# Optimization experiments

Hardware: AMD Instinct MI355X
Metric: run time of the kernel (lower is better)

The kernel has to match this reference:

```python
import jax, jax.numpy as jnp
import numpy as np

B, N, DIN, DOUT, T = 16384, 128, 64, 64, 16

def setup_inputs() -> dict:
    key = jax.random.key(0)
    k1, k2, k3, k4, k5 = jax.random.split(key, 5)
    input = jax.random.normal(k1, (B, N, DIN), dtype=jnp.float32)
    g = jax.random.uniform(k2, (N, N), dtype=jnp.float32)
    weight = jax.random.normal(k3, (T, DOUT, DIN), dtype=jnp.float32) * (1.0 / np.sqrt(DIN))
    bias = jax.random.normal(k4, (DOUT,), dtype=jnp.float32) * 0.01
    node_type_index = jax.random.randint(k5, (N,), 0, T, dtype=jnp.int32)
    return {"input": input, "g": g, "weight": weight, "bias": bias,
            "node_type_index": node_type_index}

def reference(input, g, weight, bias, node_type_index):
    # gather per-node weight: [N, out, in]
    w = weight[node_type_index]
    # per-node linear: input [B,N,in] x w [N,out,in] -> [B,N,out]
    h = jnp.einsum('bni,noi->bno', input, w)
    # graph aggregation: g [N,N] @ h -> [B,N,out]
    out = jnp.einsum('nm,bmo->bno', g, h)
    return out + bias
```

## Files before the change

### kernel.cpp

```cpp
#include <hip/hip_runtime.h>
#include <hip/hip_bf16.h>


#define NN   128
#define DI   64
#define DOUT 64
#define TT   16
#define NG   24
#define NCH  32

typedef __attribute__((ext_vector_type(4))) float f32x4;
typedef __attribute__((ext_vector_type(8))) short bf16x8;

__device__ __forceinline__ short f2bf(float f) {
    return __builtin_bit_cast(short, __float2bfloat16(f));
}

__device__ __forceinline__ bf16x8 cvt8(f32x4 a, f32x4 b) {
    bf16x8 r;
    r[0] = f2bf(a[0]); r[1] = f2bf(a[1]); r[2] = f2bf(a[2]); r[3] = f2bf(a[3]);
    r[4] = f2bf(b[0]); r[5] = f2bf(b[1]); r[6] = f2bf(b[2]); r[7] = f2bf(b[3]);
    return r;
}

__device__ __forceinline__ void load_lds16(const float* gp, float* lp) {
    __builtin_amdgcn_global_load_lds(
        (const __attribute__((address_space(1))) unsigned int*)gp,
        (__attribute__((address_space(3))) unsigned int*)lp, 16, 0, 0);
}

__device__ short d_wb[TT * DOUT * DI];
__device__ short d_gb[NN * NN];
__device__ int   d_gp[NG * 8];

__global__ void prep_kernel(const float* __restrict__ weight,
                            const float* __restrict__ g,
                            const int*   __restrict__ ntype) {
    const int tid    = blockIdx.x * blockDim.x + threadIdx.x;
    const int stride = gridDim.x * blockDim.x;
    for (int i = tid; i < TT * DOUT * DI; i += stride) d_wb[i] = f2bf(weight[i]);
    for (int i = tid; i < NN * NN; i += stride)        d_gb[i] = f2bf(g[i]);

    if (blockIdx.x == 0) {
        __shared__ int sh_t[NN];
        const int lt = threadIdx.x;
        if (lt < NN) sh_t[lt] = ntype[lt];
        __syncthreads();
        if (lt < TT) {
            int cnt = 0, m0 = 0;
            for (int m = NN - 1; m >= 0; --m)
                if (sh_t[m] == lt) { ++cnt; m0 = m; }
            const int ng = (cnt + 15) >> 4;
            int pfx = 0, total = 0;
            for (int t2 = 0; t2 < TT; ++t2) {
                const int v = __shfl(ng, t2, 64);
                if (t2 < lt) pfx += v;
                total += v;
            }
            const int fill = m0 * 0x01010101;
            int Gw = pfx, cur = 0, saved = 0;
            int pk[4] = {fill, fill, fill, fill};
            int gf[4] = {fill, fill, fill, fill};
            for (int m = 0; m < NN; ++m) {
                if (sh_t[m] == lt) {
                    const int w2 = cur >> 2, s8 = (cur & 3) * 8;
                    pk[w2] = (pk[w2] & ~(0xFF << s8)) | (m << s8);
                    if (++cur == 16) {
                        for (int k2 = 0; k2 < 4; ++k2) d_gp[Gw * 8 + k2] = pk[k2];
                        d_gp[Gw * 8 + 4] = lt;
                        if (!saved) { for (int k2 = 0; k2 < 4; ++k2) gf[k2] = pk[k2]; saved = 1; }
                        ++Gw; cur = 0;
                        for (int k2 = 0; k2 < 4; ++k2) pk[k2] = fill;
                    }
                }
            }
            if (cur > 0) {
                for (int k2 = 0; k2 < 4; ++k2) d_gp[Gw * 8 + k2] = pk[k2];
                d_gp[Gw * 8 + 4] = lt;
                if (!saved) { for (int k2 = 0; k2 < 4; ++k2) gf[k2] = pk[k2]; saved = 1; }
                ++Gw;
            }
            const unsigned long long msk = __ballot(ng > 0);
            if (lt == __ffsll(msk) - 1) {
                for (int gp2 = total; gp2 < NG; ++gp2) {
                    for (int k2 = 0; k2 < 4; ++k2) d_gp[gp2 * 8 + k2] = gf[k2];
                    d_gp[gp2 * 8 + 4] = lt;
                }
            }
        }
    }
}

__global__ __launch_bounds__(512, 2)
void graph_linear_main(const float* __restrict__ input,
                       const float* __restrict__ bias,
                       float* __restrict__ out)
{
    __shared__ float ibuf0[NN * DI];
    __shared__ float ibuf1[NN * DI];
    __shared__ short hbuf0[DOUT * NN];
    __shared__ short hbuf1[DOUT * NN];

    const int tid  = threadIdx.x;
    const int lane = tid & 63;
    const int wave = tid >> 6;
    const int lo   = lane & 15;
    const int hi   = lane >> 4;
    const size_t bbase = (size_t)blockIdx.x * NCH;
    const float* const inblk = input + bbase * (NN * DI);

    const int wu = __builtin_amdgcn_readfirstlane(wave);
    int mp[NG / 8][5];
#pragma unroll
    for (int it = 0; it < NG / 8; ++it) {
        const int gb = (it * 8 + wu) * 8;
#pragma unroll
        for (int k2 = 0; k2 < 5; ++k2) mp[it][k2] = d_gp[gb + k2];
    }
    bf16x8 wfr[NG / 8][8];
#pragma unroll
    for (int it = 0; it < NG / 8; ++it) {
        const short* wrow = d_wb + mp[it][4] * (DOUT * DI);
#pragma unroll
        for (int ot = 0; ot < 4; ++ot) {
            wfr[it][2 * ot]     = *(const bf16x8*)(wrow + (ot * 16 + lo) * DI + hi * 8);
            wfr[it][2 * ot + 1] = *(const bf16x8*)(wrow + (ot * 16 + lo) * DI + 32 + hi * 8);
        }
    }
    const int n2 = wave * 16 + lo;
    bf16x8 gfr[4];
#pragma unroll
    for (int cc = 0; cc < 4; ++cc)
        gfr[cc] = *(const bf16x8*)(d_gb + n2 * NN + cc * 32 + hi * 8);
    f32x4 bvv[4];
#pragma unroll
    for (int ot = 0; ot < 4; ++ot)
        bvv[ot] = *(const f32x4*)(bias + ot * 16 + hi * 4);

    auto STAGE = [&](float* dst, const float* srcrow) {
#pragma unroll
        for (int q = 0; q < 4; ++q) {
            const int ck = wave * 4 + q;
            const int U  = ck * 64 + lane;
            const int m  = U >> 4;
            const int u  = (U & 15) ^ (m & 15);
            load_lds16(srcrow + m * 64 + u * 4, dst + ck * 256);
        }
    };
    auto PHASE1 = [&](const float* ib, short* hb) {
#pragma unroll
        for (int it = 0; it < NG / 8; ++it) {
            const int p0 = mp[it][0], p1 = mp[it][1];
            const int p2 = mp[it][2], p3 = mp[it][3];
            const int ps = (lo < 8) ? ((lo < 4) ? p0 : p1) : ((lo < 12) ? p2 : p3);
            const int mA = (ps >> ((lo & 3) * 8)) & 0xFF;
            const int sA = mA & 15;
            const float* arow = ib + mA * DI;
            const f32x4 r0 = *(const f32x4*)&arow[((hi * 2)     ^ sA) * 4];
            const f32x4 r1 = *(const f32x4*)&arow[((hi * 2 + 1) ^ sA) * 4];
            const f32x4 r2 = *(const f32x4*)&arow[((hi * 2 + 8) ^ sA) * 4];
            const f32x4 r3 = *(const f32x4*)&arow[((hi * 2 + 9) ^ sA) * 4];
            const bf16x8 a0 = cvt8(r0, r1);
            const bf16x8 a1 = cvt8(r2, r3);

            f32x4 hacc[4];
#pragma unroll
            for (int ot = 0; ot < 4; ++ot) hacc[ot] = 0.0f;
#pragma unroll
            for (int ot = 0; ot < 4; ++ot) {
                hacc[ot] = __builtin_amdgcn_mfma_f32_16x16x32_bf16(a0, wfr[it][2 * ot],     hacc[ot], 0, 0, 0);
                hacc[ot] = __builtin_amdgcn_mfma_f32_16x16x32_bf16(a1, wfr[it][2 * ot + 1], hacc[ot], 0, 0, 0);
            }
            const int pst = (hi < 2) ? ((hi == 0) ? p0 : p1) : ((hi == 2) ? p2 : p3);
#pragma unroll
            for (int ot = 0; ot < 4; ++ot) {
                const int o   = ot * 16 + lo;
                const int swz = (o & 7) << 3;
#pragma unroll
                for (int j = 0; j < 4; ++j) {
                    const int mS = (pst >> (8 * j)) & 0xFF;
                    hb[o * NN + (mS ^ swz)] = f2bf(hacc[ot][j]);
                }
            }
        }
    };
    auto PHASE2 = [&](const short* hb, float* orow) {
        f32x4 acc[4];
#pragma unroll
        for (int ot = 0; ot < 4; ++ot) acc[ot] = bvv[ot];
#pragma unroll
        for (int cc = 0; cc < 4; ++cc) {
#pragma unroll
            for (int ot = 0; ot < 4; ++ot) {
                const int o   = ot * 16 + lo;
                const int pos = (cc * 32 + hi * 8) ^ ((o & 7) << 3);
                const bf16x8 hfr = *(const bf16x8*)&hb[o * NN + pos];
                acc[ot] = __builtin_amdgcn_mfma_f32_16x16x32_bf16(hfr, gfr[cc], acc[ot], 0, 0, 0);
            }
        }
#pragma unroll
        for (int ot = 0; ot < 4; ++ot)
            *(f32x4*)&orow[ot * 16 + hi * 4] = acc[ot];
    };

    STAGE(ibuf0, inblk);
    __syncthreads();
    STAGE(ibuf1, inblk + NN * DI);
    PHASE1(ibuf0, hbuf0);
    __syncthreads();

#pragma unroll 1
    for (int c = 1; c < NCH; ++c) {
        if (c + 1 < NCH)
            STAGE((c & 1) ? ibuf0 : ibuf1, inblk + (size_t)(c + 1) * (NN * DI));
        PHASE1((c & 1) ? ibuf1 : ibuf0, (c & 1) ? hbuf1 : hbuf0);
        PHASE2((c & 1) ? hbuf0 : hbuf1,
               out + ((bbase + c - 1) * NN + n2) * DOUT);
        __syncthreads();
    }
    PHASE2(hbuf1, out + ((bbase + NCH - 1) * NN + n2) * DOUT);
}

extern "C" void kernel_launch(void* const* d_in, const int* in_sizes, int n_in,
                              void* d_out, int out_size, void* d_ws, size_t ws_size,
                              hipStream_t stream) {
    const float* input  = (const float*)d_in[0];
    const float* g      = (const float*)d_in[1];
    const float* weight = (const float*)d_in[2];
    const float* bias   = (const float*)d_in[3];
    const int*   ntype  = (const int*)d_in[4];
    float* out = (float*)d_out;

    const int B = in_sizes[0] / (NN * DI);

    hipLaunchKernelGGL(prep_kernel, dim3(32), dim3(256), 0, stream, weight, g, ntype);
    hipLaunchKernelGGL(graph_linear_main, dim3(B / NCH), dim3(512), 0, stream,
                       input, bias, out);
}
```

Measured before the change: 237.8 us.

## Triple-buffer input staging with partial vmcnt waits and skip padding groups

Adds a third LDS input buffer so each chunk is prefetched three steps ahead. Full __syncthreads are replaced with explicit barriers that wait only on part of the outstanding vector-memory loads (vmcnt), so later prefetches stay in flight. Padding node groups are now marked with type -1 and skipped in phase 1, where before they recomputed a duplicate group. The extra 32KB of LDS per block may stop two 512-thread blocks fitting per CU. Near the end of the loop the staging index is clamped, which causes redundant reloads of the last chunk.

Result: slower. 271.8 us (+14.3%).

```diff
diff --git a/kernel.cpp b/kernel.cpp
--- a/kernel.cpp
+++ b/kernel.cpp
@@ -8,6 +8,7 @@
 #define TT   16
 #define NG   24
 #define NCH  32
+#define RSZ  (NN * DI)
 
 typedef __attribute__((ext_vector_type(4))) float f32x4;
 typedef __attribute__((ext_vector_type(8))) short bf16x8;
@@ -28,6 +29,13 @@
         (const __attribute__((address_space(1))) unsigned int*)gp,
         (__attribute__((address_space(3))) unsigned int*)lp, 16, 0, 0);
 }
+
+#define BARLG() do { __builtin_amdgcn_sched_barrier(0); \
+    asm volatile("s_waitcnt lgkmcnt(0)" ::: "memory"); \
+    __builtin_amdgcn_s_barrier(); __builtin_amdgcn_sched_barrier(0); } while (0)
+#define BARVM(N) do { __builtin_amdgcn_sched_barrier(0); \
+    asm volatile("s_waitcnt vmcnt(" #N ") lgkmcnt(0)" ::: "memory"); \
+    __builtin_amdgcn_s_barrier(); __builtin_amdgcn_sched_barrier(0); } while (0)
 
 __device__ short d_wb[TT * DOUT * DI];
 __device__ short d_gb[NN * NN];
@@ -58,9 +66,8 @@
                 total += v;
             }
             const int fill = m0 * 0x01010101;
-            int Gw = pfx, cur = 0, saved = 0;
+            int Gw = pfx, cur = 0;
             int pk[4] = {fill, fill, fill, fill};
-            int gf[4] = {fill, fill, fill, fill};
             for (int m = 0; m < NN; ++m) {
                 if (sh_t[m] == lt) {
                     const int w2 = cur >> 2, s8 = (cur & 3) * 8;
@@ -68,7 +75,6 @@
                     if (++cur == 16) {
                         for (int k2 = 0; k2 < 4; ++k2) d_gp[Gw * 8 + k2] = pk[k2];
                         d_gp[Gw * 8 + 4] = lt;
-                        if (!saved) { for (int k2 = 0; k2 < 4; ++k2) gf[k2] = pk[k2]; saved = 1; }
                         ++Gw; cur = 0;
                         for (int k2 = 0; k2 < 4; ++k2) pk[k2] = fill;
                     }
@@ -77,14 +83,12 @@
             if (cur > 0) {
                 for (int k2 = 0; k2 < 4; ++k2) d_gp[Gw * 8 + k2] = pk[k2];
                 d_gp[Gw * 8 + 4] = lt;
-                if (!saved) { for (int k2 = 0; k2 < 4; ++k2) gf[k2] = pk[k2]; saved = 1; }
                 ++Gw;
             }
-            const unsigned long long msk = __ballot(ng > 0);
-            if (lt == __ffsll(msk) - 1) {
+            if (lt == 0) {
                 for (int gp2 = total; gp2 < NG; ++gp2) {
-                    for (int k2 = 0; k2 < 4; ++k2) d_gp[gp2 * 8 + k2] = gf[k2];
-                    d_gp[gp2 * 8 + 4] = lt;
+                    for (int k2 = 0; k2 < 4; ++k2) d_gp[gp2 * 8 + k2] = 0;
+                    d_gp[gp2 * 8 + 4] = -1;
                 }
             }
         }
@@ -96,8 +100,9 @@
                        const float* __restrict__ bias,
                        float* __restrict__ out)
 {
-    __shared__ float ibuf0[NN * DI];
-    __shared__ float ibuf1[NN * DI];
+    __shared__ float ibuf0[RSZ];
+    __shared__ float ibuf1[RSZ];
+    __shared__ float ibuf2[RSZ];
     __shared__ short hbuf0[DOUT * NN];
     __shared__ short hbuf1[DOUT * NN];
 
@@ -107,7 +112,7 @@
     const int lo   = lane & 15;
     const int hi   = lane >> 4;
     const size_t bbase = (size_t)blockIdx.x * NCH;
-    const float* const inblk = input + bbase * (NN * DI);
+    const float* const inblk = input + bbase * RSZ;
 
     const int wu = __builtin_amdgcn_readfirstlane(wave);
     int mp[NG / 8][5];
@@ -120,7 +125,8 @@
     bf16x8 wfr[NG / 8][8];
 #pragma unroll
     for (int it = 0; it < NG / 8; ++it) {
-        const short* wrow = d_wb + mp[it][4] * (DOUT * DI);
+        const int t = (mp[it][4] < 0) ? 0 : mp[it][4];
+        const short* wrow = d_wb + t * (DOUT * DI);
 #pragma unroll
         for (int ot = 0; ot < 4; ++ot) {
             wfr[it][2 * ot]     = *(const bf16x8*)(wrow + (ot * 16 + lo) * DI + hi * 8);
@@ -150,6 +156,7 @@
     auto PHASE1 = [&](const float* ib, short* hb) {
 #pragma unroll
         for (int it = 0; it < NG / 8; ++it) {
+            if (mp[it][4] < 0) continue;
             const int p0 = mp[it][0], p1 = mp[it][1];
             const int p2 = mp[it][2], p3 = mp[it][3];
             const int ps = (lo < 8) ? ((lo < 4) ? p0 : p1) : ((lo < 12) ? p2 : p3);
@@ -204,19 +211,35 @@
     };
 
     STAGE(ibuf0, inblk);
-    __syncthreads();
-    STAGE(ibuf1, inblk + NN * DI);
+    STAGE(ibuf1, inblk + RSZ);
+    STAGE(ibuf2, inblk + 2 * RSZ);
+    BARVM(8);
+
     PHASE1(ibuf0, hbuf0);
-    __syncthreads();
+    BARLG();
+    STAGE(ibuf0, inblk + 3 * RSZ);
+    BARVM(8);
+
+    PHASE1(ibuf1, hbuf1);
+    BARLG();
+    PHASE2(hbuf0, out + ((bbase + 0) * NN + n2) * DOUT);
+    STAGE(ibuf1, inblk + 4 * RSZ);
+    BARVM(12);
 
 #pragma unroll 1
-    for (int c = 1; c < NCH; ++c) {
-        if (c + 1 < NCH)
-            STAGE((c & 1) ? ibuf0 : ibuf1, inblk + (size_t)(c + 1) * (NN * DI));
-        PHASE1((c & 1) ? ibuf1 : ibuf0, (c & 1) ? hbuf1 : hbuf0);
-        PHASE2((c & 1) ? hbuf0 : hbuf1,
-               out + ((bbase + c - 1) * NN + n2) * DOUT);
-        __syncthreads();
+    for (int c = 2; c < NCH; ++c) {
+        const int k = c % 3;
+        const float* ib = (k == 0) ? ibuf0 : ((k == 1) ? ibuf1 : ibuf2);
+        float* ibw      = (k == 0) ? ibuf0 : ((k == 1) ? ibuf1 : ibuf2);
+        short* hbw      = (c & 1) ? hbuf1 : hbuf0;
+        const short* hbr = (c & 1) ? hbuf0 : hbuf1;
+
+        PHASE1(ib, hbw);
+        BARLG();
+        PHASE2(hbr, out + ((bbase + c - 1) * NN + n2) * DOUT);
+        const int rr = (c + 3 < NCH) ? (c + 3) : (NCH - 1);
+        STAGE(ibw, inblk + (size_t)rr * RSZ);
+        BARVM(16);
     }
     PHASE2(hbuf1, out + ((bbase + NCH - 1) * NN + n2) * DOUT);
 }
@@ -231,7 +254,7 @@
     const int*   ntype  = (const int*)d_in[4];
     float* out = (float*)d_out;
 
-    const int B = in_sizes[0] / (NN * DI);
+    const int B = in_sizes[0] / RSZ;
 
     hipLaunchKernelGGL(prep_kernel, dim3(32), dim3(256), 0, stream, weight, g, ntype);
     hipLaunchKernelGGL(graph_linear_main, dim3(B / NCH), dim3(512), 0, stream,
```
